# Optimization experiments

Measured on AMD Instinct MI355X. Metric: run time of the kernel, lower is better.

The kernel has to match this reference:

```python
import jax, jax.numpy as jnp
import numpy as np

N = 2_097_152
H = 128


def _xavier(key, shape):
    fan_out, fan_in = shape
    limit = float(np.sqrt(6.0 / (fan_in + fan_out)))
    return jax.random.uniform(key, shape, jnp.float32, -limit, limit)


def setup_inputs() -> dict:
    key = jax.random.key(0)
    kg, kx, k11, k12, k21, k22 = jax.random.split(key, 6)
    return {
        "g": jax.random.randint(kg, (N,), 0, 2, dtype=jnp.int32),
        "input": jax.random.normal(kx, (N,), jnp.float32),
        "w1_1": _xavier(k11, (H, 1)), "b1_1": jnp.zeros((H,), jnp.float32),
        "w1_2": _xavier(k12, (1, H)), "b1_2": jnp.zeros((1,), jnp.float32),
        "w2_1": _xavier(k21, (H, 1)), "b2_1": jnp.zeros((H,), jnp.float32),
        "w2_2": _xavier(k22, (1, H)), "b2_2": jnp.zeros((1,), jnp.float32),
    }


def _mlp(x, w1, b1, w2, b2):
    # x: [N]; w1: [H,1]; w2: [1,H]  ->  [N]
    h = jax.nn.relu(x[:, None] * w1[:, 0][None, :] + b1)  # [N,H]
    return h @ w2[0] + b2[0]                               # [N]


def reference(g, input, w1_1, b1_1, w1_2, b1_2, w2_1, b2_1, w2_2, b2_2):
    out1 = _mlp(input, w1_1, b1_1, w1_2, b1_2)
    out2 = _mlp(input, w2_1, b2_1, w2_2, b2_2)
    zero = jnp.float32(0.0)
    # output initialized to zeros; branch 1 where g==0, branch 2 where g==1
    return jnp.where(g == 0, out1, jnp.where(g == 1, out2, zero))
```

## Files before the change

kernel.cpp:

```cpp
#include <hip/hip_runtime.h>


__global__ __launch_bounds__(256) void PredEnvHatYSep_kernel(
    const int*   __restrict__ g,
    const float* __restrict__ x,
    const float* __restrict__ w11, const float* __restrict__ b11,
    const float* __restrict__ w12, const float* __restrict__ b12,
    const float* __restrict__ w21, const float* __restrict__ b21,
    const float* __restrict__ w22, const float* __restrict__ b22,
    float* __restrict__ out, int n)
{
    __shared__ float sh_pos[4], sh_neg[4];
    __shared__ int   sh_bad[4];

    const int tid = threadIdx.x;

    {
        const int  h   = tid & 127;
        const bool br1 = tid < 128;
        const float* w1 = br1 ? w11 : w21;
        const float* w2 = br1 ? w12 : w22;
        const float* b1 = br1 ? b11 : b21;

        const float a = w1[h];
        const float p = a * w2[h];
        float pos = (a > 0.0f) ? p : 0.0f;
        float neg = (a < 0.0f) ? p : 0.0f;
        int   bad = (b1[h] != 0.0f) ? 1 : 0;

        #pragma unroll
        for (int off = 32; off; off >>= 1) {
            pos += __shfl_down(pos, off);
            neg += __shfl_down(neg, off);
            bad += __shfl_down(bad, off);
        }
        if ((tid & 63) == 0) {
            const int w = tid >> 6;
            sh_pos[w] = pos;
            sh_neg[w] = neg;
            sh_bad[w] = bad;
        }
    }
    __syncthreads();

    const float spos1 = sh_pos[0] + sh_pos[1];
    const float sneg1 = sh_neg[0] + sh_neg[1];
    const float spos2 = sh_pos[2] + sh_pos[3];
    const float sneg2 = sh_neg[2] + sh_neg[3];
    const int   nbad  = sh_bad[0] + sh_bad[1] + sh_bad[2] + sh_bad[3];
    const float c1 = b12[0];
    const float c2 = b22[0];

    const int idx  = blockIdx.x * 256 + tid;
    const int base = idx * 4;
    if (base >= n) return;

    if (base + 3 < n) {
        const int4   gv = reinterpret_cast<const int4*>(g)[idx];
        const float4 xv = reinterpret_cast<const float4*>(x)[idx];
        float4 ov;

        if (nbad == 0) {
            auto f = [&](int gi, float xi) -> float {
                const float o1 = xi * (xi > 0.0f ? spos1 : sneg1) + c1;
                const float o2 = xi * (xi > 0.0f ? spos2 : sneg2) + c2;
                return gi == 0 ? o1 : (gi == 1 ? o2 : 0.0f);
            };
            ov.x = f(gv.x, xv.x); ov.y = f(gv.y, xv.y);
            ov.z = f(gv.z, xv.z); ov.w = f(gv.w, xv.w);
        } else {
            auto f = [&](int gi, float xi) -> float {
                float acc1 = 0.0f, acc2 = 0.0f;
                for (int h = 0; h < 128; ++h) {
                    acc1 += w12[h] * fmaxf(xi * w11[h] + b11[h], 0.0f);
                    acc2 += w22[h] * fmaxf(xi * w21[h] + b21[h], 0.0f);
                }
                return gi == 0 ? acc1 + c1 : (gi == 1 ? acc2 + c2 : 0.0f);
            };
            ov.x = f(gv.x, xv.x); ov.y = f(gv.y, xv.y);
            ov.z = f(gv.z, xv.z); ov.w = f(gv.w, xv.w);
        }
        reinterpret_cast<float4*>(out)[idx] = ov;
    } else {
        for (int i = base; i < n; ++i) {
            const int   gi = g[i];
            const float xi = x[i];
            float o;
            if (nbad == 0) {
                const float o1 = xi * (xi > 0.0f ? spos1 : sneg1) + c1;
                const float o2 = xi * (xi > 0.0f ? spos2 : sneg2) + c2;
                o = gi == 0 ? o1 : (gi == 1 ? o2 : 0.0f);
            } else {
                float acc1 = 0.0f, acc2 = 0.0f;
                for (int h = 0; h < 128; ++h) {
                    acc1 += w12[h] * fmaxf(xi * w11[h] + b11[h], 0.0f);
                    acc2 += w22[h] * fmaxf(xi * w21[h] + b21[h], 0.0f);
                }
                o = gi == 0 ? acc1 + c1 : (gi == 1 ? acc2 + c2 : 0.0f);
            }
            out[i] = o;
        }
    }
}

extern "C" void kernel_launch(void* const* d_in, const int* in_sizes, int n_in,
                              void* d_out, int out_size, void* d_ws, size_t ws_size,
                              hipStream_t stream) {
    const int*   g   = (const int*)  d_in[0];
    const float* x   = (const float*)d_in[1];
    const float* w11 = (const float*)d_in[2];
    const float* b11 = (const float*)d_in[3];
    const float* w12 = (const float*)d_in[4];
    const float* b12 = (const float*)d_in[5];
    const float* w21 = (const float*)d_in[6];
    const float* b21 = (const float*)d_in[7];
    const float* w22 = (const float*)d_in[8];
    const float* b22 = (const float*)d_in[9];
    float* out = (float*)d_out;

    const int n = in_sizes[1];
    const int blocks = (n + 1023) / 1024;

    PredEnvHatYSep_kernel<<<blocks, 256, 0, stream>>>(
        g, x, w11, b11, w12, b12, w21, b21, w22, b22, out, n);
}
```

Baseline: 10.10 us.

## Use per-wave weight reduction, drop shared memory sync, process two vectors per thread

Each wavefront now reduces the full 128-wide weight products by itself: every lane reads two entries, and an xor-shuffle butterfly plus __any combine them. This removes the shared-memory staging and the __syncthreads barrier. Each thread now handles two float4 groups, halving the block count, and the global loads for g and x are issued before the weight reduction so their latency can overlap it. In exchange, every wave repeats the reduction for both branches, and the tail is handled by block 0.

```diff
diff --git a/kernel.cpp b/kernel.cpp
--- a/kernel.cpp
+++ b/kernel.cpp
@@ -10,95 +10,84 @@
     const float* __restrict__ w22, const float* __restrict__ b22,
     float* __restrict__ out, int n)
 {
-    __shared__ float sh_pos[4], sh_neg[4];
-    __shared__ int   sh_bad[4];
+    const int tid  = threadIdx.x;
+    const int lane = tid & 63;
 
-    const int tid = threadIdx.x;
+    const int ng = n >> 2;
+    const int i0 = blockIdx.x * 512 + tid;
+    const int i1 = i0 + 256;
+    const bool v0 = i0 < ng;
+    const bool v1 = i1 < ng;
 
-    {
-        const int  h   = tid & 127;
-        const bool br1 = tid < 128;
-        const float* w1 = br1 ? w11 : w21;
-        const float* w2 = br1 ? w12 : w22;
-        const float* b1 = br1 ? b11 : b21;
+    int4   g0 = {0,0,0,0}, g1 = {0,0,0,0};
+    float4 x0 = {0,0,0,0}, x1 = {0,0,0,0};
+    if (v0) { g0 = reinterpret_cast<const int4*>(g)[i0];
+              x0 = reinterpret_cast<const float4*>(x)[i0]; }
+    if (v1) { g1 = reinterpret_cast<const int4*>(g)[i1];
+              x1 = reinterpret_cast<const float4*>(x)[i1]; }
 
-        const float a = w1[h];
-        const float p = a * w2[h];
-        float pos = (a > 0.0f) ? p : 0.0f;
-        float neg = (a < 0.0f) ? p : 0.0f;
-        int   bad = (b1[h] != 0.0f) ? 1 : 0;
+    const float a0 = w11[lane], a1 = w11[lane + 64];
+    const float c0 = w21[lane], c1w = w21[lane + 64];
+    const float p0 = a0 * w12[lane], p1 = a1 * w12[lane + 64];
+    const float q0 = c0 * w22[lane], q1 = c1w * w22[lane + 64];
 
-        #pragma unroll
-        for (int off = 32; off; off >>= 1) {
-            pos += __shfl_down(pos, off);
-            neg += __shfl_down(neg, off);
-            bad += __shfl_down(bad, off);
+    float pos1 = (a0 > 0.f ? p0 : 0.f) + (a1 > 0.f ? p1 : 0.f);
+    float neg1 = (a0 < 0.f ? p0 : 0.f) + (a1 < 0.f ? p1 : 0.f);
+    float pos2 = (c0 > 0.f ? q0 : 0.f) + (c1w > 0.f ? q1 : 0.f);
+    float neg2 = (c0 < 0.f ? q0 : 0.f) + (c1w < 0.f ? q1 : 0.f);
+
+    const bool badl = (b11[lane] != 0.f) | (b11[lane + 64] != 0.f) |
+                      (b21[lane] != 0.f) | (b21[lane + 64] != 0.f);
+
+    #pragma unroll
+    for (int off = 1; off < 64; off <<= 1) {
+        pos1 += __shfl_xor(pos1, off);
+        neg1 += __shfl_xor(neg1, off);
+        pos2 += __shfl_xor(pos2, off);
+        neg2 += __shfl_xor(neg2, off);
+    }
+    const bool bad = __any(badl);
+    const float cc1 = b12[0];
+    const float cc2 = b22[0];
+
+    auto fastf = [&](int gi, float xi) -> float {
+        const bool  br1 = (gi == 0);
+        const float sp  = br1 ? pos1 : pos2;
+        const float sn  = br1 ? neg1 : neg2;
+        const float cc  = br1 ? cc1  : cc2;
+        const float o   = xi * (xi > 0.f ? sp : sn) + cc;
+        return ((unsigned)gi <= 1u) ? o : 0.f;
+    };
+    auto slowf = [&](int gi, float xi) -> float {
+        float acc1 = 0.f, acc2 = 0.f;
+        for (int h = 0; h < 128; ++h) {
+            acc1 += w12[h] * fmaxf(xi * w11[h] + b11[h], 0.f);
+            acc2 += w22[h] * fmaxf(xi * w21[h] + b21[h], 0.f);
         }
-        if ((tid & 63) == 0) {
-            const int w = tid >> 6;
-            sh_pos[w] = pos;
-            sh_neg[w] = neg;
-            sh_bad[w] = bad;
-        }
+        return gi == 0 ? acc1 + cc1 : (gi == 1 ? acc2 + cc2 : 0.f);
+    };
+
+    float4 o0, o1;
+    if (!bad) {
+        o0.x = fastf(g0.x, x0.x); o0.y = fastf(g0.y, x0.y);
+        o0.z = fastf(g0.z, x0.z); o0.w = fastf(g0.w, x0.w);
+        o1.x = fastf(g1.x, x1.x); o1.y = fastf(g1.y, x1.y);
+        o1.z = fastf(g1.z, x1.z); o1.w = fastf(g1.w, x1.w);
+    } else {
+        o0.x = slowf(g0.x, x0.x); o0.y = slowf(g0.y, x0.y);
+        o0.z = slowf(g0.z, x0.z); o0.w = slowf(g0.w, x0.w);
+        o1.x = slowf(g1.x, x1.x); o1.y = slowf(g1.y, x1.y);
+        o1.z = slowf(g1.z, x1.z); o1.w = slowf(g1.w, x1.w);
     }
-    __syncthreads();
+    if (v0) reinterpret_cast<float4*>(out)[i0] = o0;
+    if (v1) reinterpret_cast<float4*>(out)[i1] = o1;
 
-    const float spos1 = sh_pos[0] + sh_pos[1];
-    const float sneg1 = sh_neg[0] + sh_neg[1];
-    const float spos2 = sh_pos[2] + sh_pos[3];
-    const float sneg2 = sh_neg[2] + sh_neg[3];
-    const int   nbad  = sh_bad[0] + sh_bad[1] + sh_bad[2] + sh_bad[3];
-    const float c1 = b12[0];
-    const float c2 = b22[0];
-
-    const int idx  = blockIdx.x * 256 + tid;
-    const int base = idx * 4;
-    if (base >= n) return;
-
-    if (base + 3 < n) {
-        const int4   gv = reinterpret_cast<const int4*>(g)[idx];
-        const float4 xv = reinterpret_cast<const float4*>(x)[idx];
-        float4 ov;
-
-        if (nbad == 0) {
-            auto f = [&](int gi, float xi) -> float {
-                const float o1 = xi * (xi > 0.0f ? spos1 : sneg1) + c1;
-                const float o2 = xi * (xi > 0.0f ? spos2 : sneg2) + c2;
-                return gi == 0 ? o1 : (gi == 1 ? o2 : 0.0f);
-            };
-            ov.x = f(gv.x, xv.x); ov.y = f(gv.y, xv.y);
-            ov.z = f(gv.z, xv.z); ov.w = f(gv.w, xv.w);
-        } else {
-            auto f = [&](int gi, float xi) -> float {
-                float acc1 = 0.0f, acc2 = 0.0f;
-                for (int h = 0; h < 128; ++h) {
-                    acc1 += w12[h] * fmaxf(xi * w11[h] + b11[h], 0.0f);
-                    acc2 += w22[h] * fmaxf(xi * w21[h] + b21[h], 0.0f);
-                }
-                return gi == 0 ? acc1 + c1 : (gi == 1 ? acc2 + c2 : 0.0f);
-            };
-            ov.x = f(gv.x, xv.x); ov.y = f(gv.y, xv.y);
-            ov.z = f(gv.z, xv.z); ov.w = f(gv.w, xv.w);
-        }
-        reinterpret_cast<float4*>(out)[idx] = ov;
-    } else {
-        for (int i = base; i < n; ++i) {
-            const int   gi = g[i];
-            const float xi = x[i];
-            float o;
-            if (nbad == 0) {
-                const float o1 = xi * (xi > 0.0f ? spos1 : sneg1) + c1;
-                const float o2 = xi * (xi > 0.0f ? spos2 : sneg2) + c2;
-                o = gi == 0 ? o1 : (gi == 1 ? o2 : 0.0f);
-            } else {
-                float acc1 = 0.0f, acc2 = 0.0f;
-                for (int h = 0; h < 128; ++h) {
-                    acc1 += w12[h] * fmaxf(xi * w11[h] + b11[h], 0.0f);
-                    acc2 += w22[h] * fmaxf(xi * w21[h] + b21[h], 0.0f);
-                }
-                o = gi == 0 ? acc1 + c1 : (gi == 1 ? acc2 + c2 : 0.0f);
-            }
-            out[i] = o;
+    if (blockIdx.x == 0) {
+        const int t = n & 3, base = n & ~3;
+        if (tid < t) {
+            const int   gi = g[base + tid];
+            const float xi = x[base + tid];
+            out[base + tid] = bad ? slowf(gi, xi) : fastf(gi, xi);
         }
     }
 }
@@ -118,8 +107,10 @@
     const float* b22 = (const float*)d_in[9];
     float* out = (float*)d_out;
 
-    const int n = in_sizes[1];
-    const int blocks = (n + 1023) / 1024;
+    const int n  = in_sizes[1];
+    const int ng = n >> 2;
+    int blocks = (ng + 511) / 512;
+    if (blocks < 1) blocks = 1;
 
     PredEnvHatYSep_kernel<<<blocks, 256, 0, stream>>>(
         g, x, w11, b11, w12, b12, w21, b21, w22, b22, out, n);
```

Result: slower. 10.37 us (+2.6%).
